# Kernel tuning notes

Hardware: AMD Instinct MI355X
Metric: run time of the kernel (lower is better)

## Reference

```python
import jax, jax.numpy as jnp
import numpy as np

ALPHA = 0.2          # LeakyReLU negative slope
NEG_CAP = -9e15      # clamp used by the original torch.where on log(adj)


def setup_inputs() -> dict:
    key = jax.random.key(0)
    B, C, V, L, H, E = 4, 32, 1000, 12, 4, 20000
    k1, k2, k3, k4 = jax.random.split(key, 4)
    x = jax.random.normal(k1, (B, C, V, L), dtype=jnp.float32)
    # xavier_uniform-like scale with gain 1.414 (use normal for simplicity of stats)
    W = jax.random.normal(k2, (H, C, C), dtype=jnp.float32) * np.float32(1.414 * np.sqrt(2.0 / (C + C)))
    a = jax.random.normal(k3, (H, 2 * C, 1), dtype=jnp.float32) * np.float32(1.414 * np.sqrt(2.0 / (2 * C + 1)))
    # edge list: V self-loops (every row nonempty -> rowsum > 0) + random edges
    rng = np.random.default_rng(0)
    src = np.concatenate([np.arange(V), rng.integers(0, V, E - V)]).astype(np.int64)
    dst = np.concatenate([np.arange(V), rng.integers(0, V, E - V)]).astype(np.int64)
    edge_index = jnp.asarray(np.stack([src, dst]))           # [2, E]
    # edge_val = adj[edge0, edge1]; positive so log() is finite
    edge_val = jax.random.uniform(k4, (E,), dtype=jnp.float32, minval=0.05, maxval=1.0)
    return {"x": x, "W": W, "a": a, "edge_index": edge_index, "edge_val": edge_val}


def reference(x, W, a, edge_index, edge_val):
    # x: [B,C,V,L], W: [H,C,C], a: [H,2C,1], edge_index: [2,E], edge_val: [E]
    H, C = W.shape[0], W.shape[2]
    V = x.shape[2]
    e0, e1 = edge_index[0], edge_index[1]

    # h = einsum('ncvl,hcd->hndvl'): [H,B,C,V,L]
    h = jnp.einsum('bcvl,hcd->hbdvl', x, W)

    # attention score: a applied to cat(h[src], h[dst]) == a_src.h[src] + a_dst.h[dst]
    a_src, a_dst = a[:, :C, 0], a[:, C:, 0]                   # [H,C]
    s_src = jnp.einsum('hbcvl,hc->hbvl', h, a_src)            # [H,B,V,L]
    s_dst = jnp.einsum('hbcvl,hc->hbvl', h, a_dst)
    score = s_src[:, :, e0, :] + s_dst[:, :, e1, :]           # [H,B,E,L]

    edge_e = jnp.exp(-jax.nn.leaky_relu(score, ALPHA))        # [H,B,E,L]
    lv = jnp.maximum(jnp.log(edge_val), NEG_CAP)              # [E]
    edge_e = edge_e * lv[None, None, :, None]
    # (dropout is identity in eval mode)

    # e_rowsum: sparse [V,V] @ ones -> per-row sum, scatter by e0: [V,H,B,L]
    rowsum = jax.ops.segment_sum(jnp.moveaxis(edge_e, 2, 0), e0, num_segments=V)

    # h_prime numerator: scatter (edge_e * h[dst]) by e0
    hg = h[:, :, :, e1, :]                                    # [H,B,C,E,L]
    msg = edge_e[:, :, None, :, :] * hg                       # [H,B,C,E,L]
    num = jax.ops.segment_sum(jnp.moveaxis(msg, 3, 0), e0, num_segments=V)  # [V,H,B,C,L]

    h_prime = num / rowsum[:, :, :, None, :]                  # [V,H,B,C,L]
    h_avg = jnp.mean(h_prime, axis=1)                         # [V,B,C,L]
    out = jnp.transpose(h_avg, (1, 2, 0, 3))                  # [B,C,V,L]
    return jax.nn.elu(out)
```

## Files before the change

### kernel.cpp

```cpp
#include <hip/hip_runtime.h>
#include <hip/hip_bf16.h>
#include <hip/hip_fp16.h>
#include <math.h>

#define HH 4
#define BB 4
#define CC 32
#define VV 1000
#define LL 12
#define EE 20000
#define NBL (BB * LL)
#define SS (HH * NBL)
#define RCAP 128
#define LALPHA 0.2f
#define NEG_CAP_F -9000000000000000.0f

typedef unsigned int uint;
typedef unsigned short ushort;

__global__ __launch_bounds__(256) void k_h(const float* __restrict__ x,
                                           const float* __restrict__ W,
                                           const float* __restrict__ a,
                                           ushort* __restrict__ h_g,
                                           float* __restrict__ s_src,
                                           float* __restrict__ s_dst,
                                           int* __restrict__ cnt) {
  if (blockIdx.y == 0 && blockIdx.x < 4) {
    cnt[blockIdx.x * 256 + threadIdx.x] = 0;
  }

  __shared__ float W_lds[HH * CC * CC];
  __shared__ float a_lds[HH * 2 * CC];
  __shared__ float x_s[CC * 2 * LL];
  __shared__ float wa[HH][2][CC];
  const int tid = threadIdx.x;
  const int b = blockIdx.y;
  const int v0 = blockIdx.x * 2;

  {
    const float4* Wf = (const float4*)W;
    float4* Wl = (float4*)W_lds;
    for (int i = tid; i < HH * CC * CC / 4; i += 256) Wl[i] = Wf[i];
  }
  a_lds[tid] = a[tid];
#pragma unroll
  for (int k = 0; k < 3; ++k) {
    int i = k * 256 + tid;
    int ci = i / 24, r = i - ci * 24;
    x_s[i] = x[(b * CC + ci) * (VV * LL) + v0 * LL + r];
  }
  __syncthreads();

  {
    int h = tid >> 6, which = (tid >> 5) & 1, ci = tid & 31;
    float acc = 0.f;
#pragma unroll
    for (int k = 0; k < CC; ++k) {
      int c = (k + ci) & 31;
      acc = fmaf(W_lds[h * CC * CC + ci * CC + c],
                 a_lds[h * 2 * CC + which * CC + c], acc);
    }
    wa[h][which][ci] = acc;
  }
  __syncthreads();

  const int vp = tid >> 7;
  const int h = (tid >> 5) & 3;
  const int c = tid & 31;
  const int v = v0 + vp;

  int xoff = (b * CC) * (VV * LL) + v * LL;
  xoff = __builtin_amdgcn_readfirstlane(xoff);
  const float* xr = x + xoff;

  float acc[LL];
#pragma unroll
  for (int l = 0; l < LL; ++l) acc[l] = 0.f;

#pragma unroll 4
  for (int ci = 0; ci < CC; ++ci) {
    float w = W_lds[h * CC * CC + ci * CC + c];
#pragma unroll
    for (int l = 0; l < LL; ++l)
      acc[l] = fmaf(xr[ci * (VV * LL) + l], w, acc[l]);
  }

  const int slab0 = h * NBL + b * LL;
#pragma unroll
  for (int l = 0; l < LL; ++l) {
    __half hv = __float2half(acc[l]);
    h_g[((size_t)(slab0 + l) * VV + v) * CC + c] = *(ushort*)&hv;
  }

  if (tid < 192) {
    int which = tid & 1;
    int t2 = tid >> 1;
    int l = t2 % 12;
    int h2 = (t2 / 12) & 3;
    int vp2 = t2 / 48;
    float s = 0.f;
#pragma unroll
    for (int ci = 0; ci < CC; ++ci)
      s = fmaf(x_s[ci * 24 + vp2 * 12 + l], wa[h2][which][ci], s);
    int slab = h2 * NBL + b * LL + l;
    float* dp = which ? s_dst : s_src;
    dp[slab * VV + v0 + vp2] = s;
  }
}

__global__ __launch_bounds__(256) void k_scatter(const int* __restrict__ ei,
                                                 const float* __restrict__ ev,
                                                 int* __restrict__ cnt,
                                                 uint2* __restrict__ csr) {
  int e = blockIdx.x * 256 + threadIdx.x;
  if (e >= EE) return;
  int r = ei[e];
  int d = ei[EE + e];
  int pos = atomicAdd(&cnt[r], 1);
  if (pos < RCAP) {
    float lv = fmaxf(__logf(ev[e]), NEG_CAP_F);
    csr[r * RCAP + pos] = make_uint2((uint)d, __float_as_uint(lv));
  }
}

__global__ __launch_bounds__(256) void k_agg(const ushort* __restrict__ hg,
                                             const float* __restrict__ s_src,
                                             const float* __restrict__ s_dst,
                                             const int* __restrict__ cnt,
                                             const uint2* __restrict__ csr,
                                             float* __restrict__ outp) {
  __shared__ uint ed_dst[4][16];
  __shared__ float ed_ee[4][16][HH];
  const int i = blockIdx.x;
  const int xcd = i & 7;
  const int q = i >> 3;
  const int bl = xcd * 6 + q / 250;
  const int vb = q % 250;
  const int warp = threadIdx.x >> 6;
  const int v = vb * 4 + warp;
  const int lane = threadIdx.x & 63;
  const int b = bl / LL, l = bl - b * LL;

  int deg = cnt[v];
  if (deg > RCAP) deg = RCAP;
  const int rbase = v * RCAP;

  const int ha = lane >> 4;
  const int ia = lane & 15;
  const int slabA = ha * NBL + bl;
  const float ssv = s_src[slabA * VV + v];
  const float* sdbA = s_dst + slabA * VV;

  const int ii = lane >> 4;
  const int h = (lane >> 2) & 3;
  const int cg = lane & 3;

  const uint hoff = (uint)((h * NBL + bl) * (VV * CC * 2)) + (uint)(cg * 16);
  const char* hgbytes = (const char*)hg;

  float num[8];
#pragma unroll
  for (int j = 0; j < 8; ++j) num[j] = 0.f;
  float rs = 0.f;

  for (int base = 0; base < deg; base += 16) {
    int e = base + ia;
    float eev = 0.f;
    int d = 0;
    if (e < deg) {
      uint2 ent = csr[rbase + e];
      d = (int)ent.x;
      float lv = __uint_as_float(ent.y);
      float s = ssv + sdbA[d];
      float lr = s > 0.f ? s : LALPHA * s;
      eev = __expf(-lr) * lv;
    }
    ed_ee[warp][ia][ha] = eev;
    if (ha == 0) ed_dst[warp][ia] = (uint)d;

    int m = deg - base;
    if (m > 16) m = 16;
    int iters = (m + 3) >> 2;
    for (int t = 0; t < iters; ++t) {
      int idx = (t << 2) + ii;
      uint d2 = ed_dst[warp][idx];
      float eh = ed_ee[warp][idx][h];
      uint voff = (d2 << 6) + hoff;
      uint4 g = *(const uint4*)(hgbytes + voff);
      __half2 p0 = __builtin_bit_cast(__half2, g.x);
      __half2 p1 = __builtin_bit_cast(__half2, g.y);
      __half2 p2 = __builtin_bit_cast(__half2, g.z);
      __half2 p3 = __builtin_bit_cast(__half2, g.w);
      num[0] = fmaf(eh, __low2float(p0), num[0]);
      num[1] = fmaf(eh, __high2float(p0), num[1]);
      num[2] = fmaf(eh, __low2float(p1), num[2]);
      num[3] = fmaf(eh, __high2float(p1), num[3]);
      num[4] = fmaf(eh, __low2float(p2), num[4]);
      num[5] = fmaf(eh, __high2float(p2), num[5]);
      num[6] = fmaf(eh, __low2float(p3), num[6]);
      num[7] = fmaf(eh, __high2float(p3), num[7]);
      rs += eh;
    }
  }

#pragma unroll
  for (int mm = 16; mm <= 32; mm <<= 1) {
#pragma unroll
    for (int j = 0; j < 8; ++j) num[j] += __shfl_xor(num[j], mm);
    rs += __shfl_xor(rs, mm);
  }
  float inv = __frcp_rn(rs);
  float val[8];
#pragma unroll
  for (int j = 0; j < 8; ++j) val[j] = num[j] * inv;
#pragma unroll
  for (int mm = 4; mm <= 8; mm <<= 1) {
#pragma unroll
    for (int j = 0; j < 8; ++j) val[j] += __shfl_xor(val[j], mm);
  }

  if (ii == 0) {
    int j0 = 2 * h;
    float a0 = val[j0] * 0.25f;
    float a1 = val[j0 + 1] * 0.25f;
    a0 = a0 > 0.f ? a0 : expm1f(a0);
    a1 = a1 > 0.f ? a1 : expm1f(a1);
    size_t o0 = ((size_t)(b * CC + cg * 8 + j0) * VV + v) * LL + l;
    outp[o0] = a0;
    outp[o0 + (size_t)VV * LL] = a1;
  }
}

extern "C" void kernel_launch(void* const* d_in, const int* in_sizes, int n_in,
                              void* d_out, int out_size, void* d_ws, size_t ws_size,
                              hipStream_t stream) {
  const float* x = (const float*)d_in[0];
  const float* W = (const float*)d_in[1];
  const float* a = (const float*)d_in[2];
  const int* ei = (const int*)d_in[3];
  const float* ev = (const float*)d_in[4];
  float* out = (float*)d_out;
  float* ws = (float*)d_ws;

  size_t o = 0;
  ushort* h_g = (ushort*)(ws + o);  o += (size_t)SS * VV * CC / 2;
  float* s_src = ws + o;            o += SS * VV;
  float* s_dst = ws + o;            o += SS * VV;
  int* cnt = (int*)(ws + o);        o += 1024;
  uint2* csr = (uint2*)(ws + o);    o += (size_t)VV * RCAP * 2;

  dim3 gA(VV / 2, BB);
  k_h<<<gA, 256, 0, stream>>>(x, W, a, h_g, s_src, s_dst, cnt);

  k_scatter<<<(EE + 255) / 256, 256, 0, stream>>>(ei, ev, cnt, csr);

  const int nblk = NBL * (VV / 4);
  k_agg<<<nblk, 256, 0, stream>>>(h_g, s_src, s_dst, cnt, csr, out);
}
```

Before: 62.36 us.

## Fuse edge scatter into projection kernel and batch four nodes per aggregation warp

Edge CSR construction now runs in extra blocks of the projection kernel instead of a separate launch. The counter zeroing moves to a memset. The aggregation kernel is remapped so each warp processes four consecutive nodes per block across half of the vertex range, with a new block-to-(b,l) mapping intended to improve L2 locality per XCD. This removes one kernel launch but adds a memset, and the new work distribution may hurt load balance or cache affinity.

New measurement: 72.64 us. +16.5%, slower.

```diff
diff --git a/kernel.cpp b/kernel.cpp
--- a/kernel.cpp
+++ b/kernel.cpp
@@ -24,9 +24,22 @@
                                            ushort* __restrict__ h_g,
                                            float* __restrict__ s_src,
                                            float* __restrict__ s_dst,
-                                           int* __restrict__ cnt) {
-  if (blockIdx.y == 0 && blockIdx.x < 4) {
-    cnt[blockIdx.x * 256 + threadIdx.x] = 0;
+                                           int* __restrict__ cnt,
+                                           const int* __restrict__ ei,
+                                           const float* __restrict__ ev,
+                                           uint2* __restrict__ csr) {
+  if (blockIdx.x >= 500) {
+    int e = ((blockIdx.x - 500) * 4 + blockIdx.y) * 256 + threadIdx.x;
+    if (e < EE) {
+      int r = ei[e];
+      int d = ei[EE + e];
+      int pos = atomicAdd(&cnt[r], 1);
+      if (pos < RCAP) {
+        float lv = fmaxf(__logf(ev[e]), NEG_CAP_F);
+        csr[r * RCAP + pos] = make_uint2((uint)d, __float_as_uint(lv));
+      }
+    }
+    return;
   }
 
   __shared__ float W_lds[HH * CC * CC];
@@ -105,21 +118,6 @@
     int slab = h2 * NBL + b * LL + l;
     float* dp = which ? s_dst : s_src;
     dp[slab * VV + v0 + vp2] = s;
-  }
-}
-
-__global__ __launch_bounds__(256) void k_scatter(const int* __restrict__ ei,
-                                                 const float* __restrict__ ev,
-                                                 int* __restrict__ cnt,
-                                                 uint2* __restrict__ csr) {
-  int e = blockIdx.x * 256 + threadIdx.x;
-  if (e >= EE) return;
-  int r = ei[e];
-  int d = ei[EE + e];
-  int pos = atomicAdd(&cnt[r], 1);
-  if (pos < RCAP) {
-    float lv = fmaxf(__logf(ev[e]), NEG_CAP_F);
-    csr[r * RCAP + pos] = make_uint2((uint)d, __float_as_uint(lv));
   }
 }
 
@@ -131,103 +129,113 @@
                                              float* __restrict__ outp) {
   __shared__ uint ed_dst[4][16];
   __shared__ float ed_ee[4][16][HH];
-  const int i = blockIdx.x;
-  const int xcd = i & 7;
-  const int q = i >> 3;
-  const int bl = xcd * 6 + q / 250;
-  const int vb = q % 250;
+  const int blk = blockIdx.x;
+  const int slot = blk & 7;
+  const int j = blk >> 3;
+  const int b = slot >> 1, hv = slot & 1;
+  const int vc = j / 12, l = j % 12;
+  const int bl = b * LL + l;
   const int warp = threadIdx.x >> 6;
-  const int v = vb * 4 + warp;
   const int lane = threadIdx.x & 63;
-  const int b = bl / LL, l = bl - b * LL;
-
-  int deg = cnt[v];
-  if (deg > RCAP) deg = RCAP;
-  const int rbase = v * RCAP;
 
   const int ha = lane >> 4;
   const int ia = lane & 15;
-  const int slabA = ha * NBL + bl;
-  const float ssv = s_src[slabA * VV + v];
-  const float* sdbA = s_dst + slabA * VV;
-
   const int ii = lane >> 4;
   const int h = (lane >> 2) & 3;
   const int cg = lane & 3;
 
+  const int vbase = hv * 500 + vc * 16 + warp * 4;
+  const int vlim = hv * 500 + 500;
+
+  const int slabA = ha * NBL + bl;
+  const float* sdbA = s_dst + slabA * VV;
   const uint hoff = (uint)((h * NBL + bl) * (VV * CC * 2)) + (uint)(cg * 16);
   const char* hgbytes = (const char*)hg;
 
-  float num[8];
-#pragma unroll
-  for (int j = 0; j < 8; ++j) num[j] = 0.f;
-  float rs = 0.f;
-
-  for (int base = 0; base < deg; base += 16) {
-    int e = base + ia;
-    float eev = 0.f;
-    int d = 0;
-    if (e < deg) {
-      uint2 ent = csr[rbase + e];
-      d = (int)ent.x;
-      float lv = __uint_as_float(ent.y);
-      float s = ssv + sdbA[d];
-      float lr = s > 0.f ? s : LALPHA * s;
-      eev = __expf(-lr) * lv;
-    }
-    ed_ee[warp][ia][ha] = eev;
-    if (ha == 0) ed_dst[warp][ia] = (uint)d;
-
-    int m = deg - base;
-    if (m > 16) m = 16;
-    int iters = (m + 3) >> 2;
-    for (int t = 0; t < iters; ++t) {
-      int idx = (t << 2) + ii;
-      uint d2 = ed_dst[warp][idx];
-      float eh = ed_ee[warp][idx][h];
-      uint voff = (d2 << 6) + hoff;
-      uint4 g = *(const uint4*)(hgbytes + voff);
-      __half2 p0 = __builtin_bit_cast(__half2, g.x);
-      __half2 p1 = __builtin_bit_cast(__half2, g.y);
-      __half2 p2 = __builtin_bit_cast(__half2, g.z);
-      __half2 p3 = __builtin_bit_cast(__half2, g.w);
-      num[0] = fmaf(eh, __low2float(p0), num[0]);
-      num[1] = fmaf(eh, __high2float(p0), num[1]);
-      num[2] = fmaf(eh, __low2float(p1), num[2]);
-      num[3] = fmaf(eh, __high2float(p1), num[3]);
-      num[4] = fmaf(eh, __low2float(p2), num[4]);
-      num[5] = fmaf(eh, __high2float(p2), num[5]);
-      num[6] = fmaf(eh, __low2float(p3), num[6]);
-      num[7] = fmaf(eh, __high2float(p3), num[7]);
-      rs += eh;
-    }
-  }
-
-#pragma unroll
-  for (int mm = 16; mm <= 32; mm <<= 1) {
-#pragma unroll
-    for (int j = 0; j < 8; ++j) num[j] += __shfl_xor(num[j], mm);
-    rs += __shfl_xor(rs, mm);
-  }
-  float inv = __frcp_rn(rs);
-  float val[8];
-#pragma unroll
-  for (int j = 0; j < 8; ++j) val[j] = num[j] * inv;
-#pragma unroll
-  for (int mm = 4; mm <= 8; mm <<= 1) {
-#pragma unroll
-    for (int j = 0; j < 8; ++j) val[j] += __shfl_xor(val[j], mm);
-  }
-
-  if (ii == 0) {
-    int j0 = 2 * h;
-    float a0 = val[j0] * 0.25f;
-    float a1 = val[j0 + 1] * 0.25f;
-    a0 = a0 > 0.f ? a0 : expm1f(a0);
-    a1 = a1 > 0.f ? a1 : expm1f(a1);
-    size_t o0 = ((size_t)(b * CC + cg * 8 + j0) * VV + v) * LL + l;
-    outp[o0] = a0;
-    outp[o0 + (size_t)VV * LL] = a1;
+#pragma unroll 1
+  for (int k = 0; k < 4; ++k) {
+    const int v = vbase + k;
+    const bool valid = (v < vlim);
+    int deg = 0;
+    float ssv = 0.f;
+    if (valid) {
+      deg = cnt[v];
+      if (deg > RCAP) deg = RCAP;
+      ssv = s_src[slabA * VV + v];
+    }
+    const int rbase = v * RCAP;
+
+    float num[8];
+#pragma unroll
+    for (int q = 0; q < 8; ++q) num[q] = 0.f;
+    float rs = 0.f;
+
+    for (int base = 0; base < deg; base += 16) {
+      int e = base + ia;
+      float eev = 0.f;
+      int d = 0;
+      if (e < deg) {
+        uint2 ent = csr[rbase + e];
+        d = (int)ent.x;
+        float lv = __uint_as_float(ent.y);
+        float s = ssv + sdbA[d];
+        float lr = s > 0.f ? s : LALPHA * s;
+        eev = __expf(-lr) * lv;
+      }
+      ed_ee[warp][ia][ha] = eev;
+      if (ha == 0) ed_dst[warp][ia] = (uint)d;
+
+      int m = deg - base;
+      if (m > 16) m = 16;
+      int iters = (m + 3) >> 2;
+      for (int t = 0; t < iters; ++t) {
+        int idx = (t << 2) + ii;
+        uint d2 = ed_dst[warp][idx];
+        float eh = ed_ee[warp][idx][h];
+        uint voff = (d2 << 6) + hoff;
+        uint4 g = *(const uint4*)(hgbytes + voff);
+        __half2 p0 = __builtin_bit_cast(__half2, g.x);
+        __half2 p1 = __builtin_bit_cast(__half2, g.y);
+        __half2 p2 = __builtin_bit_cast(__half2, g.z);
+        __half2 p3 = __builtin_bit_cast(__half2, g.w);
+        num[0] = fmaf(eh, __low2float(p0), num[0]);
+        num[1] = fmaf(eh, __high2float(p0), num[1]);
+        num[2] = fmaf(eh, __low2float(p1), num[2]);
+        num[3] = fmaf(eh, __high2float(p1), num[3]);
+        num[4] = fmaf(eh, __low2float(p2), num[4]);
+        num[5] = fmaf(eh, __high2float(p2), num[5]);
+        num[6] = fmaf(eh, __low2float(p3), num[6]);
+        num[7] = fmaf(eh, __high2float(p3), num[7]);
+        rs += eh;
+      }
+    }
+
+#pragma unroll
+    for (int mm = 16; mm <= 32; mm <<= 1) {
+#pragma unroll
+      for (int q = 0; q < 8; ++q) num[q] += __shfl_xor(num[q], mm);
+      rs += __shfl_xor(rs, mm);
+    }
+    float inv = __frcp_rn(rs);
+    float val[8];
+#pragma unroll
+    for (int q = 0; q < 8; ++q) val[q] = num[q] * inv;
+#pragma unroll
+    for (int mm = 4; mm <= 8; mm <<= 1) {
+#pragma unroll
+      for (int q = 0; q < 8; ++q) val[q] += __shfl_xor(val[q], mm);
+    }
+
+    if (ii == 0 && valid) {
+      int j0 = 2 * h;
+      float a0 = val[j0] * 0.25f;
+      float a1 = val[j0 + 1] * 0.25f;
+      a0 = a0 > 0.f ? a0 : expm1f(a0);
+      a1 = a1 > 0.f ? a1 : expm1f(a1);
+      size_t o0 = ((size_t)(b * CC + cg * 8 + j0) * VV + v) * LL + l;
+      outp[o0] = a0;
+      outp[o0 + (size_t)VV * LL] = a1;
+    }
   }
 }
 
@@ -249,11 +257,10 @@
   int* cnt = (int*)(ws + o);        o += 1024;
   uint2* csr = (uint2*)(ws + o);    o += (size_t)VV * RCAP * 2;
 
-  dim3 gA(VV / 2, BB);
-  k_h<<<gA, 256, 0, stream>>>(x, W, a, h_g, s_src, s_dst, cnt);
-
-  k_scatter<<<(EE + 255) / 256, 256, 0, stream>>>(ei, ev, cnt, csr);
-
-  const int nblk = NBL * (VV / 4);
-  k_agg<<<nblk, 256, 0, stream>>>(h_g, s_src, s_dst, cnt, csr, out);
+  hipMemsetAsync(cnt, 0, 1024 * sizeof(int), stream);
+
+  dim3 gA(520, BB);
+  k_h<<<gA, 256, 0, stream>>>(x, W, a, h_g, s_src, s_dst, cnt, ei, ev, csr);
+
+  k_agg<<<3072, 256, 0, stream>>>(h_g, s_src, s_dst, cnt, csr, out);
 }
```

## Fuse edge scatter into projection kernel and use shuffles instead of LDS in aggregation

Applied to the files above, without the earlier changes.

Moves the CSR scatter into extra blocks of the projection kernel, so one launch is removed. The counter zeroing moves to a hipMemsetAsync ahead of that kernel, so the scatter blocks no longer race with the reset. In the aggregation kernel, edge destinations and weights are broadcast with wave shuffles instead of a shared-memory staging buffer. The leaky ReLU select also becomes an fmaxf. The memset adds a small API call in exchange for one fewer kernel launch.

After: 63.28 us. About the same (+1.5%).

```diff
diff --git a/kernel.cpp b/kernel.cpp
--- a/kernel.cpp
+++ b/kernel.cpp
@@ -24,9 +24,22 @@
                                            ushort* __restrict__ h_g,
                                            float* __restrict__ s_src,
                                            float* __restrict__ s_dst,
-                                           int* __restrict__ cnt) {
-  if (blockIdx.y == 0 && blockIdx.x < 4) {
-    cnt[blockIdx.x * 256 + threadIdx.x] = 0;
+                                           int* __restrict__ cnt,
+                                           const int* __restrict__ ei,
+                                           const float* __restrict__ ev,
+                                           uint2* __restrict__ csr) {
+  if (blockIdx.x >= 500) {
+    int e = ((blockIdx.x - 500) * 4 + blockIdx.y) * 256 + threadIdx.x;
+    if (e < EE) {
+      int r = ei[e];
+      int d = ei[EE + e];
+      int pos = atomicAdd(&cnt[r], 1);
+      if (pos < RCAP) {
+        float lv = fmaxf(__logf(ev[e]), NEG_CAP_F);
+        csr[r * RCAP + pos] = make_uint2((uint)d, __float_as_uint(lv));
+      }
+    }
+    return;
   }
 
   __shared__ float W_lds[HH * CC * CC];
@@ -108,29 +121,12 @@
   }
 }
 
-__global__ __launch_bounds__(256) void k_scatter(const int* __restrict__ ei,
-                                                 const float* __restrict__ ev,
-                                                 int* __restrict__ cnt,
-                                                 uint2* __restrict__ csr) {
-  int e = blockIdx.x * 256 + threadIdx.x;
-  if (e >= EE) return;
-  int r = ei[e];
-  int d = ei[EE + e];
-  int pos = atomicAdd(&cnt[r], 1);
-  if (pos < RCAP) {
-    float lv = fmaxf(__logf(ev[e]), NEG_CAP_F);
-    csr[r * RCAP + pos] = make_uint2((uint)d, __float_as_uint(lv));
-  }
-}
-
 __global__ __launch_bounds__(256) void k_agg(const ushort* __restrict__ hg,
                                              const float* __restrict__ s_src,
                                              const float* __restrict__ s_dst,
                                              const int* __restrict__ cnt,
                                              const uint2* __restrict__ csr,
                                              float* __restrict__ outp) {
-  __shared__ uint ed_dst[4][16];
-  __shared__ float ed_ee[4][16][HH];
   const int i = blockIdx.x;
   const int xcd = i & 7;
   const int q = i >> 3;
@@ -154,6 +150,7 @@
   const int ii = lane >> 4;
   const int h = (lane >> 2) & 3;
   const int cg = lane & 3;
+  const int ehsrc = h << 4;
 
   const uint hoff = (uint)((h * NBL + bl) * (VV * CC * 2)) + (uint)(cg * 16);
   const char* hgbytes = (const char*)hg;
@@ -172,20 +169,18 @@
       d = (int)ent.x;
       float lv = __uint_as_float(ent.y);
       float s = ssv + sdbA[d];
-      float lr = s > 0.f ? s : LALPHA * s;
+      float lr = fmaxf(s, LALPHA * s);
       eev = __expf(-lr) * lv;
     }
-    ed_ee[warp][ia][ha] = eev;
-    if (ha == 0) ed_dst[warp][ia] = (uint)d;
 
     int m = deg - base;
     if (m > 16) m = 16;
     int iters = (m + 3) >> 2;
     for (int t = 0; t < iters; ++t) {
       int idx = (t << 2) + ii;
-      uint d2 = ed_dst[warp][idx];
-      float eh = ed_ee[warp][idx][h];
-      uint voff = (d2 << 6) + hoff;
+      int d2 = __shfl(d, idx);
+      float eh = __shfl(eev, ehsrc | idx);
+      uint voff = ((uint)d2 << 6) + hoff;
       uint4 g = *(const uint4*)(hgbytes + voff);
       __half2 p0 = __builtin_bit_cast(__half2, g.x);
       __half2 p1 = __builtin_bit_cast(__half2, g.y);
@@ -249,11 +244,10 @@
   int* cnt = (int*)(ws + o);        o += 1024;
   uint2* csr = (uint2*)(ws + o);    o += (size_t)VV * RCAP * 2;
 
-  dim3 gA(VV / 2, BB);
-  k_h<<<gA, 256, 0, stream>>>(x, W, a, h_g, s_src, s_dst, cnt);
-
-  k_scatter<<<(EE + 255) / 256, 256, 0, stream>>>(ei, ev, cnt, csr);
-
-  const int nblk = NBL * (VV / 4);
-  k_agg<<<nblk, 256, 0, stream>>>(h_g, s_src, s_dst, cnt, csr, out);
+  hipMemsetAsync(cnt, 0, 1024 * sizeof(int), stream);
+
+  dim3 gA(520, BB);
+  k_h<<<gA, 256, 0, stream>>>(x, W, a, h_g, s_src, s_dst, cnt, ei, ev, csr);
+
+  k_agg<<<12000, 256, 0, stream>>>(h_g, s_src, s_dst, cnt, csr, out);
 }
```
